# Performance work log

Hardware: AMD Instinct MI355X
Metric: run time of the kernel (lower is better)

Reference implementation:

```python
import jax, jax.numpy as jnp
import numpy as np

# sizes
No, Nc, Ns, Nn, Nd = 80000, 20000, 5000, 500, 50
H, L, C = 256, 3, 1024  # hidden_dim, num_layers, NUM_CLASSES (VOCAB_SIZE=1023)
OCC_F, CHORD_F, SEC_F, NOTE_F, SD_F = 64, 32, 16, 16, 8
EPS = 1e-5


def setup_inputs() -> dict:
    key = jax.random.key(0)
    ks = iter(jax.random.split(key, 64))

    def nrm(sh, s=0.05):
        return jax.random.normal(next(ks), sh, jnp.float32) * s

    def edge(n, hi_s, hi_d):
        s = jax.random.randint(next(ks), (n,), 0, hi_s, dtype=jnp.int32)
        d = jax.random.randint(next(ks), (n,), 0, hi_d, dtype=jnp.int32)
        return jnp.stack([s, d])

    inp = {
        'x_occ': nrm((No, OCC_F), 1.0), 'x_chord': nrm((Nc, CHORD_F), 1.0),
        'x_sec': nrm((Ns, SEC_F), 1.0), 'x_note': nrm((Nn, NOTE_F), 1.0),
        'x_sd': nrm((Nd, SD_F), 1.0),
        'ei_occ_occ': edge(No, No, No),
        'ei_occ_chord': edge(No, No, Nc),
        'ei_chord_occ': edge(No, Nc, No),
        'ei_occ_sec': edge(No, No, Ns),
        'ei_sec_occ': edge(No, Ns, No),
        'ei_sec_sec': edge(Ns, Ns, Ns),
        'ei_chord_note': edge(4 * Nc, Nc, Nn),
        'ei_note_chord': edge(4 * Nc, Nn, Nc),
        'ei_chord_sd': edge(Nc, Nc, Nd),
        'ei_sd_chord': edge(Nc, Nd, Nc),
        # type-specific input projections (torch Linear: y = x @ W.T + b)
        'W_occ': nrm((H, OCC_F + CHORD_F)), 'b_occ': jnp.zeros((H,), jnp.float32),
        'W_chord': nrm((H, CHORD_F)), 'b_chord': jnp.zeros((H,), jnp.float32),
        'W_sec': nrm((H, SEC_F)), 'b_sec': jnp.zeros((H,), jnp.float32),
        'W_note': nrm((H, NOTE_F)), 'b_note': jnp.zeros((H,), jnp.float32),
        'W_sd': nrm((H, SD_F)), 'b_sd': jnp.zeros((H,), jnp.float32),
        'type_emb': nrm((5, H)),
        # per-layer SAGEConv: lin_l (on aggregated, with bias) + lin_r (on root)
        'Wl': nrm((L, H, H)), 'bl': jnp.zeros((L, H), jnp.float32),
        'Wr': nrm((L, H, H)),
        'ln_g': jnp.ones((L, H), jnp.float32), 'ln_b': jnp.zeros((L, H), jnp.float32),
        'Wc': nrm((C, H)), 'bc': jnp.zeros((C,), jnp.float32),
    }
    return inp


def _forward(x_occ, x_chord, x_sec, x_note, x_sd,
             W_occ, b_occ, W_chord, b_chord, W_sec, b_sec, W_note, b_note,
             W_sd, b_sd, type_emb, Wl, bl, Wr, ln_g, ln_b, Wc, bc, edges):
    (ei_occ_occ, ei_occ_chord, ei_chord_occ, ei_occ_sec, ei_sec_occ,
     ei_sec_sec, ei_chord_note, ei_note_chord, ei_chord_sd, ei_sd_chord) = edges

    # enrich occ inputs with chord features via scatter-set over inst_rev edges
    chord_per_occ = jnp.zeros((No, CHORD_F), x_occ.dtype)
    chord_per_occ = chord_per_occ.at[ei_chord_occ[1]].set(x_chord[ei_chord_occ[0]])
    occ_in = jnp.concatenate([x_occ, chord_per_occ], axis=1)

    h = jnp.concatenate([
        occ_in @ W_occ.T + b_occ + type_emb[0],
        x_chord @ W_chord.T + b_chord + type_emb[1],
        x_sec @ W_sec.T + b_sec + type_emb[2],
        x_note @ W_note.T + b_note + type_emb[3],
        x_sd @ W_sd.T + b_sd + type_emb[4],
    ], axis=0)  # [N, H]
    N = No + Nc + Ns + Nn + Nd
    o_occ, o_chord, o_sec, o_note, o_sd = 0, No, No + Nc, No + Nc + Ns, No + Nc + Ns + Nn

    # concatenate homogeneous edge set with node-type offsets
    pairs = [(ei_occ_occ, o_occ, o_occ), (ei_occ_chord, o_occ, o_chord),
             (ei_chord_occ, o_chord, o_occ), (ei_occ_sec, o_occ, o_sec),
             (ei_sec_occ, o_sec, o_occ), (ei_sec_sec, o_sec, o_sec),
             (ei_chord_note, o_chord, o_note), (ei_note_chord, o_note, o_chord),
             (ei_chord_sd, o_chord, o_sd), (ei_sd_chord, o_sd, o_chord)]
    src = jnp.concatenate([ei[0] + a for ei, a, _ in pairs])
    dst = jnp.concatenate([ei[1] + b for ei, _, b in pairs])

    # mean in-degree normalizer (shared across layers)
    cnt = jax.ops.segment_sum(jnp.ones_like(dst, h.dtype), dst, num_segments=N)
    inv_cnt = (1.0 / jnp.maximum(cnt, 1.0))[:, None]  # [N, 1]

    for l in range(L):
        # SAGEConv: lin_l(mean_{j->i} h_j) + lin_r(h_i)
        agg = jax.ops.segment_sum(h[src], dst, num_segments=N) * inv_cnt
        conv = agg @ Wl[l].T + bl[l] + h @ Wr[l].T
        # LayerNorm (dropout is identity in eval) + residual
        mu = conv.mean(axis=-1, keepdims=True)
        xc = conv - mu
        var = (xc * xc).mean(axis=-1, keepdims=True)
        h = xc * jax.lax.rsqrt(var + EPS) * ln_g[l] + ln_b[l] + h

    return h[:No] @ Wc.T + bc  # [N_occ, NUM_CLASSES]


def reference(x_occ, x_chord, x_sec, x_note, x_sd,
              ei_occ_occ, ei_occ_chord, ei_chord_occ, ei_occ_sec, ei_sec_occ,
              ei_sec_sec, ei_chord_note, ei_note_chord, ei_chord_sd, ei_sd_chord,
              W_occ, b_occ, W_chord, b_chord, W_sec, b_sec, W_note, b_note,
              W_sd, b_sd, type_emb, Wl, bl, Wr, ln_g, ln_b, Wc, bc):
    edges = (ei_occ_occ, ei_occ_chord, ei_chord_occ, ei_occ_sec, ei_sec_occ,
             ei_sec_sec, ei_chord_note, ei_note_chord, ei_chord_sd, ei_sd_chord)
    return _forward(x_occ, x_chord, x_sec, x_note, x_sd,
                    W_occ, b_occ, W_chord, b_chord, W_sec, b_sec, W_note, b_note,
                    W_sd, b_sd, type_emb, Wl, bl, Wr, ln_g, ln_b, Wc, bc, edges)
```

## Files before the change

### kernel.cpp

```cpp
#include <hip/hip_runtime.h>


#define kNo 80000
#define kNc 20000
#define kNs 5000
#define kNn 500
#define kNd 50
#define kN  105550
#define kH  256
#define kC  1024
#define kE  605000
#define LN_EPS 1e-5f
#define NBLK 413

typedef unsigned int u32;
typedef unsigned short ush;
typedef __attribute__((ext_vector_type(8))) short short8;
typedef __attribute__((ext_vector_type(4))) float f32x4;

__device__ __forceinline__ float b2f(ush b) {
  u32 u = ((u32)b) << 16;
  float f;
  __builtin_memcpy(&f, &u, 4);
  return f;
}
__device__ __forceinline__ ush f2b(float x) {
  u32 u;
  __builtin_memcpy(&u, &x, 4);
  u32 r = (u + 0x7fffu + ((u >> 16) & 1u)) >> 16;
  return (ush)r;
}
__device__ __forceinline__ float up_hi(u32 u) {
  u32 v = u & 0xffff0000u;
  float f;
  __builtin_memcpy(&f, &v, 4);
  return f;
}
__device__ __forceinline__ float up_lo(u32 u) {
  u32 v = u << 16;
  float f;
  __builtin_memcpy(&f, &v, 4);
  return f;
}
__device__ __forceinline__ float upk(u32 u) { return up_hi(u) + up_lo(u); }
__device__ __forceinline__ u32 pk(float x) {
  ush hi = f2b(x);
  ush lo = f2b(x - b2f(hi));
  return (((u32)hi) << 16) | (u32)lo;
}

union S8u {
  u32 w[4];
  short8 s;
};
__device__ __forceinline__ void unpk8(uint4 a, uint4 b, short8& hi, short8& lo) {
  S8u h, l;
  h.w[0] = (a.x >> 16) | (a.y & 0xffff0000u);
  h.w[1] = (a.z >> 16) | (a.w & 0xffff0000u);
  h.w[2] = (b.x >> 16) | (b.y & 0xffff0000u);
  h.w[3] = (b.z >> 16) | (b.w & 0xffff0000u);
  l.w[0] = (a.x & 0xffffu) | (a.y << 16);
  l.w[1] = (a.z & 0xffffu) | (a.w << 16);
  l.w[2] = (b.x & 0xffffu) | (b.y << 16);
  l.w[3] = (b.z & 0xffffu) | (b.w << 16);
  hi = h.s;
  lo = l.s;
}

__device__ __forceinline__ void gload16(const void* g, void* l) {
  __builtin_amdgcn_global_load_lds((const __attribute__((address_space(1))) u32*)g,
                                   (__attribute__((address_space(3))) u32*)l, 16, 0, 0);
}

struct EdgeTab {
  const int* p[10];
  int n[10], so[10], dofs[10], cum[11];
};

__global__ __launch_bounds__(256) void k_edges(EdgeTab t, int* __restrict__ src_g,
                                               int* __restrict__ dst_g,
                                               int* __restrict__ cnt) {
  int e = blockIdx.x * 256 + threadIdx.x;
  if (e >= kE) return;
  int s = 0;
#pragma unroll
  for (int i = 1; i < 10; ++i) s += (e >= t.cum[i]) ? 1 : 0;
  int j = e - t.cum[s];
  const int* p = t.p[s];
  int src = p[j] + t.so[s];
  int dst = p[t.n[s] + j] + t.dofs[s];
  src_g[e] = src;
  dst_g[e] = dst;
  atomicAdd(&cnt[dst], 1);
}

__global__ __launch_bounds__(256) void k_winner(const int* __restrict__ ei,
                                                int* __restrict__ winner) {
  int e = blockIdx.x * 256 + threadIdx.x;
  if (e >= kNo) return;
  atomicMax(&winner[ei[kNo + e]], e);
}

__global__ __launch_bounds__(256) void k_scat(const int* __restrict__ ei,
                                              const int* __restrict__ winner,
                                              const float* __restrict__ xch,
                                              float* __restrict__ cpo) {
  int tid = blockIdx.x * 256 + threadIdx.x;
  if (tid >= kNo * 8) return;
  int e = tid >> 3, q = tid & 7;
  int d = ei[kNo + e];
  if (winner[d] == e) {
    int s = ei[e];
    ((float4*)cpo)[d * 8 + q] = ((const float4*)xch)[s * 8 + q];
  }
}

__global__ __launch_bounds__(256) void k_pack2(const float* __restrict__ A1, int K1,
                                               const float* __restrict__ A2, int K2,
                                               int Kp, u32* __restrict__ Xp, int M) {
  int tid = blockIdx.x * 256 + threadIdx.x;
  if (tid >= M * Kp) return;
  int r = tid / Kp, c = tid - r * Kp;
  float v = 0.f;
  if (c < K1) v = A1[(size_t)r * K1 + c];
  else if (c < K1 + K2) v = A2[(size_t)r * K2 + (c - K1)];
  Xp[tid] = pk(v);
}

__global__ __launch_bounds__(256) void k_wsplit(const float* __restrict__ W, int K,
                                                int Kp, ush* __restrict__ hi,
                                                ush* __restrict__ lo) {
  int tid = blockIdx.x * 256 + threadIdx.x;
  if (tid >= 256 * Kp) return;
  int r = tid / Kp, c = tid - r * Kp;
  float v = (c < K) ? W[(size_t)r * K + c] : 0.f;
  ush h = f2b(v);
  hi[tid] = h;
  lo[tid] = f2b(v - b2f(h));
}

struct PArgs {
  const u32* Xp;
  const ush* Wh;
  const ush* Wlo;
  const float* bias;
  const float* emb;
  u32* out;
  int M, Kp;
};

__global__ __launch_bounds__(256) void k_pmg(PArgs g) {
  __shared__ u32 Apk[64 * 32];
  __shared__ ush Wht[256 * 32];
  __shared__ ush Wlt[256 * 32];

  const int tid = threadIdx.x;
  const int wv = tid >> 6;
  const int l = tid & 63;
  const int fr = l & 15, fk = l >> 4;
  const int r0 = blockIdx.x * 64;

  const int ac0 = (((fk * 2) ^ (fr & 7)) * 4);
  const int ac1 = (((fk * 2 + 1) ^ (fr & 7)) * 4);
  const int wc8 = ((fk ^ (fr & 3)) * 8);

  const int arow = tid >> 3, ach = tid & 7;
  const int wrow = tid >> 2, wch = tid & 3;
  const int ar0g = (r0 + arow < g.M) ? (r0 + arow) : (g.M - 1);
  const int ar1g = (r0 + arow + 32 < g.M) ? (r0 + arow + 32) : (g.M - 1);
  const int aswz = (ach ^ (arow & 7)) * 4;
  const int wswz = (wch ^ (wrow & 3)) * 8;

  f32x4 acc[4][4];
#pragma unroll
  for (int m = 0; m < 4; ++m)
#pragma unroll
    for (int n = 0; n < 4; ++n) acc[m][n] = (f32x4)(0.f);

  const u32* a0 = g.Xp + (size_t)ar0g * g.Kp + aswz;
  const u32* a1 = g.Xp + (size_t)ar1g * g.Kp + aswz;
  const ush* wh = g.Wh + (size_t)wrow * g.Kp + wswz;
  const ush* wl = g.Wlo + (size_t)wrow * g.Kp + wswz;

#pragma unroll 1
  for (int kc = 0; kc < g.Kp; kc += 32) {
    __syncthreads();
    gload16(a0 + kc, Apk + tid * 4);
    gload16(a1 + kc, Apk + (tid + 256) * 4);
#pragma unroll
    for (int i = 0; i < 4; ++i) {
      gload16(wh + (size_t)i * 64 * g.Kp + kc, Wht + (tid + i * 256) * 8);
      gload16(wl + (size_t)i * 64 * g.Kp + kc, Wlt + (tid + i * 256) * 8);
    }
    __syncthreads();

    short8 ah[4], al[4], whf[4], wlf[4];
#pragma unroll
    for (int m = 0; m < 4; ++m) {
      const uint4 x = *(const uint4*)(Apk + (m * 16 + fr) * 32 + ac0);
      const uint4 y = *(const uint4*)(Apk + (m * 16 + fr) * 32 + ac1);
      unpk8(x, y, ah[m], al[m]);
    }
#pragma unroll
    for (int n = 0; n < 4; ++n) {
      whf[n] = *(const short8*)(Wht + (wv * 64 + n * 16 + fr) * 32 + wc8);
      wlf[n] = *(const short8*)(Wlt + (wv * 64 + n * 16 + fr) * 32 + wc8);
    }
#pragma unroll
    for (int m = 0; m < 4; ++m)
#pragma unroll
      for (int n = 0; n < 4; ++n) {
        acc[m][n] = __builtin_amdgcn_mfma_f32_16x16x32_bf16(ah[m], whf[n],
                                                            acc[m][n], 0, 0, 0);
        acc[m][n] = __builtin_amdgcn_mfma_f32_16x16x32_bf16(ah[m], wlf[n],
                                                            acc[m][n], 0, 0, 0);
        acc[m][n] = __builtin_amdgcn_mfma_f32_16x16x32_bf16(al[m], whf[n],
                                                            acc[m][n], 0, 0, 0);
      }
  }

  float bn[4];
#pragma unroll
  for (int n = 0; n < 4; ++n) {
    const int col = wv * 64 + n * 16 + fr;
    bn[n] = g.bias[col] + g.emb[col];
  }
#pragma unroll
  for (int m = 0; m < 4; ++m)
#pragma unroll
    for (int j = 0; j < 4; ++j) {
      const int ri = r0 + m * 16 + fk * 4 + j;
      if (ri < g.M) {
        u32* op = g.out + (size_t)ri * kH + wv * 64 + fr;
#pragma unroll
        for (int n = 0; n < 4; ++n) op[n * 16] = pk(acc[m][n][j] + bn[n]);
      }
    }
}

__global__ __launch_bounds__(256) void k_scan1(const int* __restrict__ cnt,
                                               int* __restrict__ bsum) {
  __shared__ int s[256];
  int b = blockIdx.x, t = threadIdx.x;
  int i = b * 256 + t;
  s[t] = (i < kN) ? cnt[i] : 0;
  __syncthreads();
  for (int off = 128; off; off >>= 1) {
    if (t < off) s[t] += s[t + off];
    __syncthreads();
  }
  if (t == 0) bsum[b] = s[0];
}

__global__ __launch_bounds__(512) void k_scan2(const int* __restrict__ bsum,
                                               int* __restrict__ bscan) {
  __shared__ int s[512];
  int t = threadIdx.x;
  s[t] = (t < NBLK) ? bsum[t] : 0;
  __syncthreads();
  for (int off = 1; off < 512; off <<= 1) {
    int v = (t >= off) ? s[t - off] : 0;
    __syncthreads();
    s[t] += v;
    __syncthreads();
  }
  if (t < NBLK) bscan[t] = s[t];
}

__global__ __launch_bounds__(256) void k_scan3(const int* __restrict__ cnt,
                                               const int* __restrict__ bscan,
                                               int* __restrict__ rowptr,
                                               int* __restrict__ cursor,
                                               float* __restrict__ inv) {
  __shared__ int s[256];
  int b = blockIdx.x, t = threadIdx.x;
  int i = b * 256 + t;
  int v = (i < kN) ? cnt[i] : 0;
  s[t] = v;
  __syncthreads();
  for (int off = 1; off < 256; off <<= 1) {
    int u = (t >= off) ? s[t - off] : 0;
    __syncthreads();
    s[t] += u;
    __syncthreads();
  }
  int incl = s[t];
  int base = (b > 0) ? bscan[b - 1] : 0;
  int excl = base + incl - v;
  if (i < kN) {
    rowptr[i] = excl;
    cursor[i] = excl;
    inv[i] = 1.f / (float)(v > 1 ? v : 1);
    if (i == kN - 1) rowptr[kN] = excl + v;
  }
}

__global__ __launch_bounds__(256) void k_fill(const int* __restrict__ src_g,
                                              const int* __restrict__ dst_g,
                                              int* __restrict__ cursor,
                                              int* __restrict__ csr_src) {
  int e = blockIdx.x * 256 + threadIdx.x;
  if (e >= kE) return;
  int d = dst_g[e];
  int slot = atomicAdd(&cursor[d], 1);
  csr_src[slot] = src_g[e];
}

__global__ __launch_bounds__(256) void k_agg(const u32* __restrict__ hpk,
                                             const int* __restrict__ rowptr,
                                             const int* __restrict__ csr_src,
                                             const float* __restrict__ inv,
                                             u32* __restrict__ apk) {
  const int wave = threadIdx.x >> 6, lane = threadIdx.x & 63;
  const int node = blockIdx.x * 4 + wave;
  if (node >= kN) return;
  const int jb = rowptr[node], je = rowptr[node + 1];
  float a0 = 0.f, a1 = 0.f, a2 = 0.f, a3 = 0.f;
  const int coff = lane * 4;

  int j = jb;
  while (j < je) {
    const int batch = min(je - j, 64);
    const int myi = (lane < batch) ? csr_src[j + lane] : 0;
    int t = 0;
    for (; t + 4 <= batch; t += 4) {
      const int s0 = __shfl(myi, t);
      const int s1 = __shfl(myi, t + 1);
      const int s2 = __shfl(myi, t + 2);
      const int s3 = __shfl(myi, t + 3);
      const uint4 v0 = *(const uint4*)(hpk + (size_t)s0 * kH + coff);
      const uint4 v1 = *(const uint4*)(hpk + (size_t)s1 * kH + coff);
      const uint4 v2 = *(const uint4*)(hpk + (size_t)s2 * kH + coff);
      const uint4 v3 = *(const uint4*)(hpk + (size_t)s3 * kH + coff);
      a0 += upk(v0.x) + upk(v1.x) + upk(v2.x) + upk(v3.x);
      a1 += upk(v0.y) + upk(v1.y) + upk(v2.y) + upk(v3.y);
      a2 += upk(v0.z) + upk(v1.z) + upk(v2.z) + upk(v3.z);
      a3 += upk(v0.w) + upk(v1.w) + upk(v2.w) + upk(v3.w);
    }
    for (; t < batch; ++t) {
      const int s0 = __shfl(myi, t);
      const uint4 v0 = *(const uint4*)(hpk + (size_t)s0 * kH + coff);
      a0 += upk(v0.x);
      a1 += upk(v0.y);
      a2 += upk(v0.z);
      a3 += upk(v0.w);
    }
    j += batch;
  }
  const float ic = inv[node];
  uint4 o;
  o.x = pk(a0 * ic);
  o.y = pk(a1 * ic);
  o.z = pk(a2 * ic);
  o.w = pk(a3 * ic);
  *(uint4*)(apk + (size_t)node * kH + coff) = o;
}

struct GArgs {
  const u32* A[2];
  const ush* Wh[2];
  const ush* Wl[2];
  const float* bias;
  const float* lng;
  const float* lnb;
  const u32* rpk;
  float* outf;
  u32* opk;
  int M, npass, ostride;
};

template <bool LN>
__global__ __launch_bounds__(256) void k_mg(GArgs g) {
  __shared__ u32 Apk[64 * 32];
  __shared__ ush Wht[256 * 32];
  __shared__ ush Wlt[256 * 32];
  __shared__ float redS[4][64];
  __shared__ float redQ[4][64];

  const int tid = threadIdx.x;
  const int wv = tid >> 6;
  const int l = tid & 63;
  const int fr = l & 15, fk = l >> 4;
  const int r0 = blockIdx.x * 64;
  const int cb = blockIdx.y << 8;

  const int ac0 = (((fk * 2) ^ (fr & 7)) * 4);
  const int ac1 = (((fk * 2 + 1) ^ (fr & 7)) * 4);
  const int wc8 = ((fk ^ (fr & 3)) * 8);

  const int arow = tid >> 3;
  const int ach = tid & 7;
  const int wrow = tid >> 2;
  const int wch = tid & 3;
  const int ar0g = (r0 + arow < g.M) ? (r0 + arow) : (g.M - 1);
  const int ar1g = (r0 + arow + 32 < g.M) ? (r0 + arow + 32) : (g.M - 1);
  const int aswz = (ach ^ (arow & 7)) * 4;
  const int wswz = (wch ^ (wrow & 3)) * 8;

  f32x4 acc[4][4];
#pragma unroll
  for (int m = 0; m < 4; ++m)
#pragma unroll
    for (int n = 0; n < 4; ++n) acc[m][n] = (f32x4)(0.f);

#pragma unroll 1
  for (int p = 0; p < g.npass; ++p) {
    const u32* a0 = g.A[p] + (size_t)ar0g * kH + aswz;
    const u32* a1 = g.A[p] + (size_t)ar1g * kH + aswz;
    const ush* wh = g.Wh[p] + (size_t)(cb + wrow) * kH + wswz;
    const ush* wl = g.Wl[p] + (size_t)(cb + wrow) * kH + wswz;
#pragma unroll 1
    for (int kc = 0; kc < kH; kc += 32) {
      __syncthreads();
      gload16(a0 + kc, Apk + tid * 4);
      gload16(a1 + kc, Apk + (tid + 256) * 4);
#pragma unroll
      for (int i = 0; i < 4; ++i) {
        gload16(wh + (size_t)i * 64 * kH + kc, Wht + (tid + i * 256) * 8);
        gload16(wl + (size_t)i * 64 * kH + kc, Wlt + (tid + i * 256) * 8);
      }
      __syncthreads();

      short8 ah[4], al[4], whf[4], wlf[4];
#pragma unroll
      for (int m = 0; m < 4; ++m) {
        const uint4 x = *(const uint4*)(Apk + (m * 16 + fr) * 32 + ac0);
        const uint4 y = *(const uint4*)(Apk + (m * 16 + fr) * 32 + ac1);
        unpk8(x, y, ah[m], al[m]);
      }
#pragma unroll
      for (int n = 0; n < 4; ++n) {
        whf[n] = *(const short8*)(Wht + (wv * 64 + n * 16 + fr) * 32 + wc8);
        wlf[n] = *(const short8*)(Wlt + (wv * 64 + n * 16 + fr) * 32 + wc8);
      }
#pragma unroll
      for (int m = 0; m < 4; ++m)
#pragma unroll
        for (int n = 0; n < 4; ++n) {
          acc[m][n] = __builtin_amdgcn_mfma_f32_16x16x32_bf16(ah[m], whf[n],
                                                              acc[m][n], 0, 0, 0);
          acc[m][n] = __builtin_amdgcn_mfma_f32_16x16x32_bf16(ah[m], wlf[n],
                                                              acc[m][n], 0, 0, 0);
          acc[m][n] = __builtin_amdgcn_mfma_f32_16x16x32_bf16(al[m], whf[n],
                                                              acc[m][n], 0, 0, 0);
        }
    }
  }

  float bn[4];
#pragma unroll
  for (int n = 0; n < 4; ++n) bn[n] = g.bias[cb + wv * 64 + n * 16 + fr];
#pragma unroll
  for (int m = 0; m < 4; ++m)
#pragma unroll
    for (int n = 0; n < 4; ++n)
#pragma unroll
      for (int j = 0; j < 4; ++j) acc[m][n][j] += bn[n];

  if (LN) {
#pragma unroll
    for (int m = 0; m < 4; ++m)
#pragma unroll
      for (int j = 0; j < 4; ++j) {
        float s = acc[m][0][j] + acc[m][1][j] + acc[m][2][j] + acc[m][3][j];
        float q = acc[m][0][j] * acc[m][0][j] + acc[m][1][j] * acc[m][1][j] +
                  acc[m][2][j] * acc[m][2][j] + acc[m][3][j] * acc[m][3][j];
#pragma unroll
        for (int d = 1; d < 16; d <<= 1) {
          s += __shfl_xor(s, d);
          q += __shfl_xor(q, d);
        }
        if (fr == 0) {
          redS[wv][m * 16 + fk * 4 + j] = s;
          redQ[wv][m * 16 + fk * 4 + j] = q;
        }
      }
    __syncthreads();
    float gg[4], eb[4];
#pragma unroll
    for (int n = 0; n < 4; ++n) {
      gg[n] = g.lng[wv * 64 + n * 16 + fr];
      eb[n] = g.lnb[wv * 64 + n * 16 + fr];
    }
#pragma unroll
    for (int m = 0; m < 4; ++m)
#pragma unroll
      for (int j = 0; j < 4; ++j) {
        const int rt = m * 16 + fk * 4 + j;
        const float S = redS[0][rt] + redS[1][rt] + redS[2][rt] + redS[3][rt];
        const float Q = redQ[0][rt] + redQ[1][rt] + redQ[2][rt] + redQ[3][rt];
        const float mu = S * (1.f / 256.f);
        float var = Q * (1.f / 256.f) - mu * mu;
        var = var > 0.f ? var : 0.f;
        const float rstd = rsqrtf(var + LN_EPS);
        const int ri = r0 + rt;
        if (ri < g.M) {
          const size_t base = (size_t)ri * kH + wv * 64 + fr;
#pragma unroll
          for (int n = 0; n < 4; ++n) {
            const size_t ix = base + n * 16;
            const float res = upk(g.rpk[ix]);
            const float y = (acc[m][n][j] - mu) * rstd * gg[n] + eb[n] + res;
            g.opk[ix] = pk(y);
          }
        }
      }
  } else {
#pragma unroll
    for (int m = 0; m < 4; ++m)
#pragma unroll
      for (int j = 0; j < 4; ++j) {
        const int ri = r0 + m * 16 + fk * 4 + j;
        if (ri < g.M) {
          float* op = g.outf + (size_t)ri * g.ostride + cb + wv * 64 + fr;
#pragma unroll
          for (int n = 0; n < 4; ++n) op[n * 16] = acc[m][n][j];
        }
      }
  }
}

__global__ __launch_bounds__(256) void k_split(const float* __restrict__ s,
                                               ush* __restrict__ hi,
                                               ush* __restrict__ lo, int n) {
  int i = blockIdx.x * 256 + threadIdx.x;
  if (i >= n) return;
  float v = s[i];
  ush h = f2b(v);
  hi[i] = h;
  lo[i] = f2b(v - b2f(h));
}

extern "C" void kernel_launch(void* const* d_in, const int* in_sizes, int n_in,
                              void* d_out, int out_size, void* d_ws, size_t ws_size,
                              hipStream_t stream) {
  (void)in_sizes; (void)n_in; (void)out_size; (void)ws_size;
  const float* x_occ    = (const float*)d_in[0];
  const float* x_chord  = (const float*)d_in[1];
  const float* x_sec    = (const float*)d_in[2];
  const float* x_note   = (const float*)d_in[3];
  const float* x_sd     = (const float*)d_in[4];
  const int* ei[10];
  for (int i = 0; i < 10; ++i) ei[i] = (const int*)d_in[5 + i];
  const float* W_occ    = (const float*)d_in[15];
  const float* b_occ    = (const float*)d_in[16];
  const float* W_chord  = (const float*)d_in[17];
  const float* b_chord  = (const float*)d_in[18];
  const float* W_sec    = (const float*)d_in[19];
  const float* b_sec    = (const float*)d_in[20];
  const float* W_note   = (const float*)d_in[21];
  const float* b_note   = (const float*)d_in[22];
  const float* W_sd     = (const float*)d_in[23];
  const float* b_sd     = (const float*)d_in[24];
  const float* type_emb = (const float*)d_in[25];
  const float* Wl       = (const float*)d_in[26];
  const float* bl       = (const float*)d_in[27];
  const float* Wr       = (const float*)d_in[28];
  const float* ln_g     = (const float*)d_in[29];
  const float* ln_b     = (const float*)d_in[30];
  const float* Wc       = (const float*)d_in[31];
  const float* bc       = (const float*)d_in[32];

  char* base = (char*)d_ws;
  u32* h_pk   = (u32*)(base);
  char* R = base + 108083200u;
  u32* agg_pk = (u32*)R;
  char* wb = base + 216166400u;
  ush* Wl_hi = (ush*)(wb);
  ush* Wl_lo = (ush*)(wb + 393216u);
  ush* Wr_hi = (ush*)(wb + 786432u);
  ush* Wr_lo = (ush*)(wb + 1179648u);
  ush* Wc_hi = (ush*)(wb + 1572864u);
  ush* Wc_lo = (ush*)(wb + 2097152u);
  ush* Wo_hi = (ush*)(wb + 2621440u);
  ush* Wo_lo = (ush*)(wb + 2670592u);
  ush* Wch_hi = (ush*)(wb + 2719744u);
  ush* Wch_lo = (ush*)(wb + 2736128u);
  ush* Wse_hi = (ush*)(wb + 2752512u);
  ush* Wse_lo = (ush*)(wb + 2768896u);
  ush* Wnt_hi = (ush*)(wb + 2785280u);
  ush* Wnt_lo = (ush*)(wb + 2801664u);
  ush* Wsd_hi = (ush*)(wb + 2818048u);
  ush* Wsd_lo = (ush*)(wb + 2834432u);
  int* ip = (int*)(wb + 2850816u);
  int* csr_src = ip;
  int* cnt     = ip + 605000;
  int* rowptr  = ip + 710550;
  int* cursor  = ip + 816101;
  float* inv   = (float*)(ip + 921651);
  int* bsum    = ip + 1027201;
  int* bscan   = ip + 1027614;
  float* cpo  = (float*)(R);
  int* winner = (int*)(R + 10240000u);
  int* src_g  = (int*)(R + 10560000u);
  int* dst_g  = (int*)(R + 12980000u);
  u32* Xp_occ = (u32*)(R + 16000000u);
  u32* Xp_ch  = (u32*)(R + 46720000u);
  u32* Xp_se  = (u32*)(R + 49280000u);
  u32* Xp_nt  = (u32*)(R + 49920000u);
  u32* Xp_sd  = (u32*)(R + 49984000u);

  hipMemsetAsync(winner, 0xFF, kNo * 4, stream);
  hipMemsetAsync(cpo, 0, (size_t)kNo * 32 * 4, stream);
  hipMemsetAsync(cnt, 0, kN * 4, stream);

  k_split<<<768, 256, 0, stream>>>(Wl, Wl_hi, Wl_lo, 3 * kH * kH);
  k_split<<<768, 256, 0, stream>>>(Wr, Wr_hi, Wr_lo, 3 * kH * kH);
  k_split<<<1024, 256, 0, stream>>>(Wc, Wc_hi, Wc_lo, kC * kH);

  k_wsplit<<<(256 * 96 + 255) / 256, 256, 0, stream>>>(W_occ, 96, 96, Wo_hi, Wo_lo);
  k_wsplit<<<32, 256, 0, stream>>>(W_chord, 32, 32, Wch_hi, Wch_lo);
  k_wsplit<<<32, 256, 0, stream>>>(W_sec, 16, 32, Wse_hi, Wse_lo);
  k_wsplit<<<32, 256, 0, stream>>>(W_note, 16, 32, Wnt_hi, Wnt_lo);
  k_wsplit<<<32, 256, 0, stream>>>(W_sd, 8, 32, Wsd_hi, Wsd_lo);

  k_winner<<<(kNo + 255) / 256, 256, 0, stream>>>(ei[2], winner);
  k_scat<<<(kNo * 8) / 256, 256, 0, stream>>>(ei[2], winner, x_chord, cpo);

  k_pack2<<<(kNo * 96 + 255) / 256, 256, 0, stream>>>(x_occ, 64, cpo, 32, 96, Xp_occ, kNo);
  k_pack2<<<(kNc * 32 + 255) / 256, 256, 0, stream>>>(x_chord, 32, nullptr, 0, 32, Xp_ch, kNc);
  k_pack2<<<(kNs * 32 + 255) / 256, 256, 0, stream>>>(x_sec, 16, nullptr, 0, 32, Xp_se, kNs);
  k_pack2<<<(kNn * 32 + 255) / 256, 256, 0, stream>>>(x_note, 16, nullptr, 0, 32, Xp_nt, kNn);
  k_pack2<<<(kNd * 32 + 255) / 256, 256, 0, stream>>>(x_sd, 8, nullptr, 0, 32, Xp_sd, kNd);

  {
    PArgs p{};
    p.Xp = Xp_occ; p.Wh = Wo_hi; p.Wlo = Wo_lo; p.bias = b_occ;
    p.emb = type_emb + 0 * kH; p.out = h_pk; p.M = kNo; p.Kp = 96;
    k_pmg<<<(kNo + 63) / 64, 256, 0, stream>>>(p);
    p.Xp = Xp_ch; p.Wh = Wch_hi; p.Wlo = Wch_lo; p.bias = b_chord;
    p.emb = type_emb + 1 * kH; p.out = h_pk + (size_t)kNo * kH; p.M = kNc; p.Kp = 32;
    k_pmg<<<(kNc + 63) / 64, 256, 0, stream>>>(p);
    p.Xp = Xp_se; p.Wh = Wse_hi; p.Wlo = Wse_lo; p.bias = b_sec;
    p.emb = type_emb + 2 * kH; p.out = h_pk + (size_t)100000 * kH; p.M = kNs; p.Kp = 32;
    k_pmg<<<(kNs + 63) / 64, 256, 0, stream>>>(p);
    p.Xp = Xp_nt; p.Wh = Wnt_hi; p.Wlo = Wnt_lo; p.bias = b_note;
    p.emb = type_emb + 3 * kH; p.out = h_pk + (size_t)105000 * kH; p.M = kNn; p.Kp = 32;
    k_pmg<<<(kNn + 63) / 64, 256, 0, stream>>>(p);
    p.Xp = Xp_sd; p.Wh = Wsd_hi; p.Wlo = Wsd_lo; p.bias = b_sd;
    p.emb = type_emb + 4 * kH; p.out = h_pk + (size_t)105500 * kH; p.M = kNd; p.Kp = 32;
    k_pmg<<<(kNd + 63) / 64, 256, 0, stream>>>(p);
  }

  EdgeTab tab;
  const int ns_[10]  = {80000, 80000, 80000, 80000, 80000, 5000, 80000, 80000, 20000, 20000};
  const int sos_[10] = {0, 0, 80000, 0, 100000, 100000, 80000, 105000, 80000, 105500};
  const int dos_[10] = {0, 80000, 0, 100000, 0, 100000, 105000, 80000, 105500, 80000};
  int cum = 0;
  for (int i = 0; i < 10; ++i) {
    tab.p[i] = ei[i]; tab.n[i] = ns_[i]; tab.so[i] = sos_[i]; tab.dofs[i] = dos_[i];
    tab.cum[i] = cum; cum += ns_[i];
  }
  tab.cum[10] = cum;

  k_edges<<<(kE + 255) / 256, 256, 0, stream>>>(tab, src_g, dst_g, cnt);
  k_scan1<<<NBLK, 256, 0, stream>>>(cnt, bsum);
  k_scan2<<<1, 512, 0, stream>>>(bsum, bscan);
  k_scan3<<<NBLK, 256, 0, stream>>>(cnt, bscan, rowptr, cursor, inv);
  k_fill<<<(kE + 255) / 256, 256, 0, stream>>>(src_g, dst_g, cursor, csr_src);

  for (int l = 0; l < 3; ++l) {
    k_agg<<<(kN + 3) / 4, 256, 0, stream>>>(h_pk, rowptr, csr_src, inv, agg_pk);
    GArgs a{};
    const size_t off = (size_t)l * kH * kH;
    a.A[0] = agg_pk;      a.A[1] = h_pk;
    a.Wh[0] = Wl_hi + off; a.Wh[1] = Wr_hi + off;
    a.Wl[0] = Wl_lo + off; a.Wl[1] = Wr_lo + off;
    a.bias = bl + l * kH;
    a.lng = ln_g + l * kH;
    a.lnb = ln_b + l * kH;
    a.rpk = h_pk;
    a.outf = nullptr;
    a.opk = h_pk;
    a.M = kN; a.npass = 2; a.ostride = kH;
    k_mg<true><<<dim3((kN + 63) / 64, 1), 256, 0, stream>>>(a);
  }

  GArgs c{};
  c.A[0] = h_pk;
  c.Wh[0] = Wc_hi;
  c.Wl[0] = Wc_lo;
  c.bias = bc;
  c.rpk = nullptr;
  c.outf = (float*)d_out;
  c.opk = nullptr;
  c.M = kNo; c.npass = 1; c.ostride = kC;
  k_mg<false><<<dim3(kNo / 64, 4), 256, 0, stream>>>(c);
}
```

Measured before the change: 1.311 ms.

## Double GEMM row tile to 128 and widen aggregation gather unroll to eight

Result: slower. 1.602 ms (+22.2%).

```diff
diff --git a/kernel.cpp b/kernel.cpp
--- a/kernel.cpp
+++ b/kernel.cpp
@@ -323,19 +323,21 @@
     const int batch = min(je - j, 64);
     const int myi = (lane < batch) ? csr_src[j + lane] : 0;
     int t = 0;
-    for (; t + 4 <= batch; t += 4) {
-      const int s0 = __shfl(myi, t);
-      const int s1 = __shfl(myi, t + 1);
-      const int s2 = __shfl(myi, t + 2);
-      const int s3 = __shfl(myi, t + 3);
-      const uint4 v0 = *(const uint4*)(hpk + (size_t)s0 * kH + coff);
-      const uint4 v1 = *(const uint4*)(hpk + (size_t)s1 * kH + coff);
-      const uint4 v2 = *(const uint4*)(hpk + (size_t)s2 * kH + coff);
-      const uint4 v3 = *(const uint4*)(hpk + (size_t)s3 * kH + coff);
-      a0 += upk(v0.x) + upk(v1.x) + upk(v2.x) + upk(v3.x);
-      a1 += upk(v0.y) + upk(v1.y) + upk(v2.y) + upk(v3.y);
-      a2 += upk(v0.z) + upk(v1.z) + upk(v2.z) + upk(v3.z);
-      a3 += upk(v0.w) + upk(v1.w) + upk(v2.w) + upk(v3.w);
+    for (; t + 8 <= batch; t += 8) {
+      int s[8];
+#pragma unroll
+      for (int q = 0; q < 8; ++q) s[q] = __shfl(myi, t + q);
+      uint4 v[8];
+#pragma unroll
+      for (int q = 0; q < 8; ++q)
+        v[q] = *(const uint4*)(hpk + (size_t)s[q] * kH + coff);
+#pragma unroll
+      for (int q = 0; q < 8; ++q) {
+        a0 += upk(v[q].x);
+        a1 += upk(v[q].y);
+        a2 += upk(v[q].z);
+        a3 += upk(v[q].w);
+      }
     }
     for (; t < batch; ++t) {
       const int s0 = __shfl(myi, t);
@@ -371,79 +373,80 @@
 
 template <bool LN>
 __global__ __launch_bounds__(256) void k_mg(GArgs g) {
-  __shared__ u32 Apk[64 * 32];
+  __shared__ u32 Apk[128 * 32];
   __shared__ ush Wht[256 * 32];
   __shared__ ush Wlt[256 * 32];
-  __shared__ float redS[4][64];
-  __shared__ float redQ[4][64];
+  __shared__ float redS[4][128];
+  __shared__ float redQ[4][128];
 
   const int tid = threadIdx.x;
   const int wv = tid >> 6;
   const int l = tid & 63;
   const int fr = l & 15, fk = l >> 4;
-  const int r0 = blockIdx.x * 64;
+  const int r0 = blockIdx.x * 128;
   const int cb = blockIdx.y << 8;
 
   const int ac0 = (((fk * 2) ^ (fr & 7)) * 4);
   const int ac1 = (((fk * 2 + 1) ^ (fr & 7)) * 4);
-  const int wc8 = ((fk ^ (fr & 3)) * 8);
-
-  const int arow = tid >> 3;
-  const int ach = tid & 7;
-  const int wrow = tid >> 2;
-  const int wch = tid & 3;
-  const int ar0g = (r0 + arow < g.M) ? (r0 + arow) : (g.M - 1);
-  const int ar1g = (r0 + arow + 32 < g.M) ? (r0 + arow + 32) : (g.M - 1);
-  const int aswz = (ach ^ (arow & 7)) * 4;
-  const int wswz = (wch ^ (wrow & 3)) * 8;
-
-  f32x4 acc[4][4];
-#pragma unroll
-  for (int m = 0; m < 4; ++m)
+  const int wc8 = ((fk ^ (fr >> 2)) * 8);
+
+  const int abase = tid >> 3;
+  const int aswz = ((tid & 7) ^ (abase & 7)) * 4;
+  const int wbase = tid >> 2;
+  const int wswz = ((tid & 3) ^ ((tid >> 4) & 3)) * 8;
+  int arg[4];
+#pragma unroll
+  for (int i = 0; i < 4; ++i) {
+    int r = r0 + i * 32 + abase;
+    arg[i] = (r < g.M) ? r : (g.M - 1);
+  }
+
+  f32x4 acc[8][4];
+#pragma unroll
+  for (int m = 0; m < 8; ++m)
 #pragma unroll
     for (int n = 0; n < 4; ++n) acc[m][n] = (f32x4)(0.f);
 
 #pragma unroll 1
   for (int p = 0; p < g.npass; ++p) {
-    const u32* a0 = g.A[p] + (size_t)ar0g * kH + aswz;
-    const u32* a1 = g.A[p] + (size_t)ar1g * kH + aswz;
-    const ush* wh = g.Wh[p] + (size_t)(cb + wrow) * kH + wswz;
-    const ush* wl = g.Wl[p] + (size_t)(cb + wrow) * kH + wswz;
+    const u32* aP = g.A[p];
+    const ush* whP = g.Wh[p] + (size_t)(cb + wbase) * kH + wswz;
+    const ush* wlP = g.Wl[p] + (size_t)(cb + wbase) * kH + wswz;
 #pragma unroll 1
     for (int kc = 0; kc < kH; kc += 32) {
       __syncthreads();
-      gload16(a0 + kc, Apk + tid * 4);
-      gload16(a1 + kc, Apk + (tid + 256) * 4);
+#pragma unroll
+      for (int i = 0; i < 4; ++i)
+        gload16(aP + (size_t)arg[i] * kH + aswz + kc, Apk + (i * 256 + tid) * 4);
 #pragma unroll
       for (int i = 0; i < 4; ++i) {
-        gload16(wh + (size_t)i * 64 * kH + kc, Wht + (tid + i * 256) * 8);
-        gload16(wl + (size_t)i * 64 * kH + kc, Wlt + (tid + i * 256) * 8);
+        gload16(whP + (size_t)i * 64 * kH + kc, Wht + (i * 256 + tid) * 8);
+        gload16(wlP + (size_t)i * 64 * kH + kc, Wlt + (i * 256 + tid) * 8);
       }
       __syncthreads();
 
-      short8 ah[4], al[4], whf[4], wlf[4];
-#pragma unroll
-      for (int m = 0; m < 4; ++m) {
-        const uint4 x = *(const uint4*)(Apk + (m * 16 + fr) * 32 + ac0);
-        const uint4 y = *(const uint4*)(Apk + (m * 16 + fr) * 32 + ac1);
-        unpk8(x, y, ah[m], al[m]);
-      }
+      short8 whf[4], wlf[4];
 #pragma unroll
       for (int n = 0; n < 4; ++n) {
         whf[n] = *(const short8*)(Wht + (wv * 64 + n * 16 + fr) * 32 + wc8);
         wlf[n] = *(const short8*)(Wlt + (wv * 64 + n * 16 + fr) * 32 + wc8);
       }
 #pragma unroll
-      for (int m = 0; m < 4; ++m)
+      for (int m = 0; m < 8; ++m) {
+        const uint4 x = *(const uint4*)(Apk + (m * 16 + fr) * 32 + ac0);
+        const uint4 y = *(const uint4*)(Apk + (m * 16 + fr) * 32 + ac1);
+        short8 ah, al;
+        unpk8(x, y, ah, al);
 #pragma unroll
         for (int n = 0; n < 4; ++n) {
-          acc[m][n] = __builtin_amdgcn_mfma_f32_16x16x32_bf16(ah[m], whf[n],
+          acc[m][n] = __builtin_amdgcn_mfma_f32_16x16x32_bf16(ah, whf[n],
                                                               acc[m][n], 0, 0, 0);
-          acc[m][n] = __builtin_amdgcn_mfma_f32_16x16x32_bf16(ah[m], wlf[n],
+          acc[m][n] = __builtin_amdgcn_mfma_f32_16x16x32_bf16(ah, wlf[n],
                                                               acc[m][n], 0, 0, 0);
-          acc[m][n] = __builtin_amdgcn_mfma_f32_16x16x32_bf16(al[m], whf[n],
+          acc[m][n] = __builtin_amdgcn_mfma_f32_16x16x32_bf16(al, whf[n],
                                                               acc[m][n], 0, 0, 0);
         }
+      }
     }
   }
 
@@ -451,7 +454,7 @@
 #pragma unroll
   for (int n = 0; n < 4; ++n) bn[n] = g.bias[cb + wv * 64 + n * 16 + fr];
 #pragma unroll
-  for (int m = 0; m < 4; ++m)
+  for (int m = 0; m < 8; ++m)
 #pragma unroll
     for (int n = 0; n < 4; ++n)
 #pragma unroll
@@ -459,7 +462,7 @@
 
   if (LN) {
 #pragma unroll
-    for (int m = 0; m < 4; ++m)
+    for (int m = 0; m < 8; ++m)
 #pragma unroll
       for (int j = 0; j < 4; ++j) {
         float s = acc[m][0][j] + acc[m][1][j] + acc[m][2][j] + acc[m][3][j];
@@ -483,7 +486,7 @@
       eb[n] = g.lnb[wv * 64 + n * 16 + fr];
     }
 #pragma unroll
-    for (int m = 0; m < 4; ++m)
+    for (int m = 0; m < 8; ++m)
 #pragma unroll
       for (int j = 0; j < 4; ++j) {
         const int rt = m * 16 + fk * 4 + j;
@@ -507,7 +510,7 @@
       }
   } else {
 #pragma unroll
-    for (int m = 0; m < 4; ++m)
+    for (int m = 0; m < 8; ++m)
 #pragma unroll
       for (int j = 0; j < 4; ++j) {
         const int ri = r0 + m * 16 + fk * 4 + j;
@@ -673,7 +676,7 @@
     a.outf = nullptr;
     a.opk = h_pk;
     a.M = kN; a.npass = 2; a.ostride = kH;
-    k_mg<true><<<dim3((kN + 63) / 64, 1), 256, 0, stream>>>(a);
+    k_mg<true><<<dim3((kN + 127) / 128, 1), 256, 0, stream>>>(a);
   }
 
   GArgs c{};
@@ -685,5 +688,5 @@
   c.outf = (float*)d_out;
   c.opk = nullptr;
   c.M = kNo; c.npass = 1; c.ostride = kC;
-  k_mg<false><<<dim3(kNo / 64, 4), 256, 0, stream>>>(c);
-}
+  k_mg<false><<<dim3(kNo / 128, 4), 256, 0, stream>>>(c);
+}
```

## Aggregate four nodes per wave and linearize classifier GEMM grid for row reuse

Applied to the files above, without the earlier changes.

Result: slower. 2.838 ms (+116.4%).

```diff
diff --git a/kernel.cpp b/kernel.cpp
--- a/kernel.cpp
+++ b/kernel.cpp
@@ -312,48 +312,64 @@
                                              const float* __restrict__ inv,
                                              u32* __restrict__ apk) {
   const int wave = threadIdx.x >> 6, lane = threadIdx.x & 63;
-  const int node = blockIdx.x * 4 + wave;
-  if (node >= kN) return;
-  const int jb = rowptr[node], je = rowptr[node + 1];
-  float a0 = 0.f, a1 = 0.f, a2 = 0.f, a3 = 0.f;
+  const int nb = blockIdx.x * 16 + wave * 4;
+  if (nb >= kN) return;
   const int coff = lane * 4;
 
-  int j = jb;
-  while (j < je) {
-    const int batch = min(je - j, 64);
-    const int myi = (lane < batch) ? csr_src[j + lane] : 0;
-    int t = 0;
-    for (; t + 4 <= batch; t += 4) {
-      const int s0 = __shfl(myi, t);
-      const int s1 = __shfl(myi, t + 1);
-      const int s2 = __shfl(myi, t + 2);
-      const int s3 = __shfl(myi, t + 3);
-      const uint4 v0 = *(const uint4*)(hpk + (size_t)s0 * kH + coff);
-      const uint4 v1 = *(const uint4*)(hpk + (size_t)s1 * kH + coff);
-      const uint4 v2 = *(const uint4*)(hpk + (size_t)s2 * kH + coff);
-      const uint4 v3 = *(const uint4*)(hpk + (size_t)s3 * kH + coff);
-      a0 += upk(v0.x) + upk(v1.x) + upk(v2.x) + upk(v3.x);
-      a1 += upk(v0.y) + upk(v1.y) + upk(v2.y) + upk(v3.y);
-      a2 += upk(v0.z) + upk(v1.z) + upk(v2.z) + upk(v3.z);
-      a3 += upk(v0.w) + upk(v1.w) + upk(v2.w) + upk(v3.w);
-    }
-    for (; t < batch; ++t) {
-      const int s0 = __shfl(myi, t);
-      const uint4 v0 = *(const uint4*)(hpk + (size_t)s0 * kH + coff);
-      a0 += upk(v0.x);
-      a1 += upk(v0.y);
-      a2 += upk(v0.z);
-      a3 += upk(v0.w);
-    }
-    j += batch;
-  }
-  const float ic = inv[node];
-  uint4 o;
-  o.x = pk(a0 * ic);
-  o.y = pk(a1 * ic);
-  o.z = pk(a2 * ic);
-  o.w = pk(a3 * ic);
-  *(uint4*)(apk + (size_t)node * kH + coff) = o;
+  int jb[4], dg[4];
+#pragma unroll
+  for (int q = 0; q < 4; ++q) {
+    const int node = nb + q;
+    if (node < kN) {
+      jb[q] = rowptr[node];
+      dg[q] = rowptr[node + 1] - jb[q];
+    } else {
+      jb[q] = 0;
+      dg[q] = 0;
+    }
+  }
+  float ax[4] = {0.f, 0.f, 0.f, 0.f};
+  float ay[4] = {0.f, 0.f, 0.f, 0.f};
+  float az[4] = {0.f, 0.f, 0.f, 0.f};
+  float aw[4] = {0.f, 0.f, 0.f, 0.f};
+
+  const int maxd = max(max(dg[0], dg[1]), max(dg[2], dg[3]));
+
+  for (int j0 = 0; j0 < maxd; j0 += 64) {
+    int my[4];
+#pragma unroll
+    for (int q = 0; q < 4; ++q)
+      my[q] = (j0 + lane < dg[q]) ? csr_src[jb[q] + j0 + lane] : 0;
+    const int bend = min(maxd - j0, 64);
+#pragma unroll 4
+    for (int t = 0; t < bend; ++t) {
+#pragma unroll
+      for (int q = 0; q < 4; ++q) {
+        if (j0 + t < dg[q]) {
+          const int s = __shfl(my[q], t);
+          const uint4 v = *(const uint4*)(hpk + (size_t)s * kH + coff);
+          ax[q] += upk(v.x);
+          ay[q] += upk(v.y);
+          az[q] += upk(v.z);
+          aw[q] += upk(v.w);
+        }
+      }
+    }
+  }
+
+#pragma unroll
+  for (int q = 0; q < 4; ++q) {
+    const int node = nb + q;
+    if (node < kN) {
+      const float ic = inv[node];
+      uint4 o;
+      o.x = pk(ax[q] * ic);
+      o.y = pk(ay[q] * ic);
+      o.z = pk(az[q] * ic);
+      o.w = pk(aw[q] * ic);
+      *(uint4*)(apk + (size_t)node * kH + coff) = o;
+    }
+  }
 }
 
 struct GArgs {
@@ -381,8 +397,17 @@
   const int wv = tid >> 6;
   const int l = tid & 63;
   const int fr = l & 15, fk = l >> 4;
-  const int r0 = blockIdx.x * 64;
-  const int cb = blockIdx.y << 8;
+
+  int bx, by;
+  if (LN) {
+    bx = blockIdx.x;
+    by = 0;
+  } else {
+    bx = blockIdx.x >> 2;
+    by = blockIdx.x & 3;
+  }
+  const int r0 = bx * 64;
+  const int cb = by << 8;
 
   const int ac0 = (((fk * 2) ^ (fr & 7)) * 4);
   const int ac1 = (((fk * 2 + 1) ^ (fr & 7)) * 4);
@@ -660,7 +685,7 @@
   k_fill<<<(kE + 255) / 256, 256, 0, stream>>>(src_g, dst_g, cursor, csr_src);
 
   for (int l = 0; l < 3; ++l) {
-    k_agg<<<(kN + 3) / 4, 256, 0, stream>>>(h_pk, rowptr, csr_src, inv, agg_pk);
+    k_agg<<<(kN + 15) / 16, 256, 0, stream>>>(h_pk, rowptr, csr_src, inv, agg_pk);
     GArgs a{};
     const size_t off = (size_t)l * kH * kH;
     a.A[0] = agg_pk;      a.A[1] = h_pk;
@@ -685,5 +710,5 @@
   c.outf = (float*)d_out;
   c.opk = nullptr;
   c.M = kNo; c.npass = 1; c.ostride = kC;
-  k_mg<false><<<dim3(kNo / 64, 4), 256, 0, stream>>>(c);
-}
+  k_mg<false><<<(kNo / 64) * 4, 256, 0, stream>>>(c);
+}
```
